# Kernel optimization log

Measured on AMD Instinct MI355X. Metric: run time of the kernel, lower is better.

The kernel has to match this reference:

```python
import jax, jax.numpy as jnp
import numpy as np
from math import ceil, log2

LEVELS = 6
N = 4096
DB4 = np.array([0.23037781330885523, 0.7148465705525415, 0.6308807679295904,
                -0.02798376941698385, -0.18703481171888114, 0.030841381835986965,
                0.032883011666982945, -0.010597401784997278], dtype=np.float32)


def setup_inputs() -> dict:
    key = jax.random.key(0)
    x = jax.random.normal(key, (N, N), dtype=jnp.float32)
    # learned filter bank: scaling.repeat(levels*2, 1)
    scaling = jnp.tile(jnp.asarray(DB4), (LEVELS * 2, 1))
    return {
        "x": x,
        "scaling": scaling,
        "alpha": jnp.float32(10.0),
        "b_plus": jnp.float32(2.0),
        "b_minus": jnp.float32(1.0),
    }


def compute_wavelet(h):
    # g_k = flip(h); odd indices negated
    g = jnp.flip(h, -1)
    sign = jnp.where(jnp.arange(g.shape[-1]) % 2 == 1, -1.0, 1.0).astype(g.dtype)
    return g * sign


def convolve(x, f, transpose=False):
    # circular convolution (or correlation if transpose) along last axis via FFT,
    # exactly as torch rfft/irfft with n=input_length
    L = x.shape[-1]
    fa = jnp.fft.rfft(x, axis=-1)
    fb = jnp.fft.rfft(f, n=L)
    if transpose:
        fb = jnp.conj(fb)
    return jnp.fft.irfft(fa * fb, n=L, axis=-1)


def forward_layer(x, h):
    w = compute_wavelet(h)
    return convolve(x, w)[:, ::2], convolve(x, h)[:, ::2]


def backward_layer(d, a, h):
    w = compute_wavelet(h)
    fd = jnp.zeros((d.shape[0], d.shape[1] * 2), d.dtype).at[:, ::2].set(d)
    fa = jnp.zeros((a.shape[0], a.shape[1] * 2), a.dtype).at[:, ::2].set(a)
    return convolve(fd, w, transpose=True) + convolve(fa, h, transpose=True)


def forward2d(x, hH, hV):
    d, a = forward_layer(x, hH)
    hh, hl = forward_layer(d.T, hV)
    hh, hl = hh.T, hl.T
    lh, ll = forward_layer(a.T, hV)
    lh, ll = lh.T, ll.T
    return (hh, hl, lh), ll


def backward2d(hh, hl, lh, ll, hH, hV):
    h = backward_layer(hh.T, hl.T, hV).T
    l = backward_layer(lh.T, ll.T, hV).T
    return backward_layer(h, l, hH)


def _despawn(x, scaling, alpha, b_plus, b_minus):
    n, m = x.shape
    pn = 2 ** ceil(log2(n)) - n
    pm = 2 ** ceil(log2(m)) - m
    xp = jnp.pad(x, ((0, pn), (0, pm)), mode="edge") if (pn or pm) else x

    approx = xp
    coeffs = []
    for lev in range(LEVELS):
        dets, approx = forward2d(approx, scaling[lev], scaling[lev + 1])
        coeffs.append(dets)

    def thr(t):
        return t * (jax.nn.sigmoid(alpha * (t - b_plus)) + jax.nn.sigmoid(-alpha * (t + b_minus)))

    filt = [tuple(thr(c) for c in tup) for tup in coeffs] + [thr(approx)]

    a = filt[-1]
    for lev in reversed(range(LEVELS)):
        hh, hl, lh = filt[lev]
        a = backward2d(hh, hl, lh, a, scaling[lev], scaling[lev + 1])

    flat = jnp.concatenate(
        [jnp.concatenate(tup, axis=-1).reshape(-1) for tup in filt[:-1]]
        + [filt[-1].reshape(-1)]
    )
    return a[:n, :m], flat


def reference(x, scaling, alpha, b_plus, b_minus):
    return _despawn(x, scaling, alpha, b_plus, b_minus)
```

## Files before the change

kernel.cpp:

```cpp
#include <hip/hip_runtime.h>
#include <hip/hip_bf16.h>


__device__ __forceinline__ float thrf(float t, float alpha, float bp, float bm) {
    float s1 = 1.0f / (1.0f + __expf(-alpha * (t - bp)));
    float s2 = 1.0f / (1.0f + __expf( alpha * (t + bm)));
    return t * (s1 + s2);
}

__device__ __forceinline__ void load_filt(const float* __restrict__ filt,
                                          float (&h)[8], float (&w)[8]) {
#pragma unroll
    for (int k = 0; k < 8; ++k) h[k] = filt[k];
#pragma unroll
    for (int k = 0; k < 8; ++k) w[k] = (k & 1) ? -h[7 - k] : h[7 - k];
}

__global__ __launch_bounds__(256) void fwd_fused(
    const float* __restrict__ X, int s, int sh,
    float* __restrict__ flat, float* __restrict__ All,
    const float* __restrict__ filt_row, const float* __restrict__ filt_col,
    const float* __restrict__ ap, const float* __restrict__ bpp,
    const float* __restrict__ bmp) {
    __shared__ float xs[72][73];
    __shared__ float Ds[72][33];
    __shared__ float As[72][33];
    const int tid = threadIdx.x;
    const int j0 = blockIdx.x * 32, i0 = blockIdx.y * 32;
    float hr[8], wr[8], hc[8], wc[8];
    load_filt(filt_row, hr, wr);
    load_filt(filt_col, hc, wc);
    const int sm = s - 1;
    for (int idx = tid; idx < 72 * 72; idx += 256) {
        int rr = idx / 72, cc = idx - rr * 72;
        int gr = (2 * i0 - 7 + rr) & sm;
        int gc = (2 * j0 - 7 + cc) & sm;
        xs[rr][cc] = X[(size_t)gr * s + gc];
    }
    __syncthreads();
    for (int idx = tid; idx < 72 * 32; idx += 256) {
        int rr = idx >> 5, j = idx & 31;
        float d = 0.f, a = 0.f;
#pragma unroll
        for (int k = 0; k < 8; ++k) {
            float v = xs[rr][2 * j + 7 - k];
            d += wr[k] * v;
            a += hr[k] * v;
        }
        Ds[rr][j] = d;
        As[rr][j] = a;
    }
    __syncthreads();
    const float alpha = *ap, bp = *bpp, bm = *bmp;
    for (int idx = tid; idx < 32 * 32; idx += 256) {
        int i = idx >> 5, j = idx & 31;
        float hh = 0.f, hl = 0.f, lh = 0.f, ll = 0.f;
#pragma unroll
        for (int k = 0; k < 8; ++k) {
            float dv = Ds[2 * i + 7 - k][j];
            float av = As[2 * i + 7 - k][j];
            hh += wc[k] * dv;
            hl += hc[k] * dv;
            lh += wc[k] * av;
            ll += hc[k] * av;
        }
        size_t ro = (size_t)(i0 + i) * (3 * sh) + (j0 + j);
        flat[ro]          = thrf(hh, alpha, bp, bm);
        flat[ro + sh]     = thrf(hl, alpha, bp, bm);
        flat[ro + 2 * sh] = thrf(lh, alpha, bp, bm);
        All[(size_t)(i0 + i) * sh + (j0 + j)] = ll;
    }
}

__global__ void thr_kernel(const float* __restrict__ in, float* __restrict__ out,
                           int n, const float* __restrict__ ap,
                           const float* __restrict__ bpp,
                           const float* __restrict__ bmp) {
    int idx = blockIdx.x * blockDim.x + threadIdx.x;
    if (idx >= n) return;
    out[idx] = thrf(in[idx], *ap, *bpp, *bmp);
}

__global__ __launch_bounds__(256) void inv_fused(
    const float* __restrict__ flatl, const float* __restrict__ a, int astride,
    int sc, float* __restrict__ outp, int ostride,
    const float* __restrict__ filt_col, const float* __restrict__ filt_row) {
    __shared__ float hhs[36][37], hls[36][37], lhs[36][37], as_[36][37];
    __shared__ float Hs[64][37], Ls[64][37];
    const int tid = threadIdx.x;
    const int m0 = blockIdx.x * 64, i0 = blockIdx.y * 64;
    float hr[8], wr[8], hc[8], wc[8];
    load_filt(filt_row, hr, wr);
    load_filt(filt_col, hc, wc);
    const int mm = sc - 1;
    const int r0 = i0 >> 1, c0 = m0 >> 1;
    const int ds = 3 * sc;
    for (int idx = tid; idx < 36 * 36; idx += 256) {
        int rr = idx / 36, cc = idx - rr * 36;
        int gr = (r0 + rr) & mm;
        int gc = (c0 + cc) & mm;
        size_t fo = (size_t)gr * ds + gc;
        hhs[rr][cc] = flatl[fo];
        hls[rr][cc] = flatl[fo + sc];
        lhs[rr][cc] = flatl[fo + 2 * sc];
        as_[rr][cc] = a[(size_t)gr * astride + gc];
    }
    __syncthreads();
    for (int idx = tid; idx < 64 * 36; idx += 256) {
        int n = idx / 36, jj = idx - (idx / 36) * 36;
        int nh = n >> 1;
        float Hv = 0.f, Lv = 0.f;
        if ((n & 1) == 0) {
#pragma unroll
            for (int t = 0; t < 4; ++t) {
                int lr = nh + t;
                Hv += wc[2 * t] * hhs[lr][jj] + hc[2 * t] * hls[lr][jj];
                Lv += wc[2 * t] * lhs[lr][jj] + hc[2 * t] * as_[lr][jj];
            }
        } else {
#pragma unroll
            for (int t = 0; t < 4; ++t) {
                int lr = nh + t + 1;
                Hv += wc[2 * t + 1] * hhs[lr][jj] + hc[2 * t + 1] * hls[lr][jj];
                Lv += wc[2 * t + 1] * lhs[lr][jj] + hc[2 * t + 1] * as_[lr][jj];
            }
        }
        Hs[n][jj] = Hv;
        Ls[n][jj] = Lv;
    }
    __syncthreads();
    for (int idx = tid; idx < 64 * 64; idx += 256) {
        int i = idx >> 6, m = idx & 63;
        int mh = m >> 1;
        float acc = 0.f;
        if ((m & 1) == 0) {
#pragma unroll
            for (int t = 0; t < 4; ++t) {
                int lc = mh + t;
                acc += wr[2 * t] * Hs[i][lc] + hr[2 * t] * Ls[i][lc];
            }
        } else {
#pragma unroll
            for (int t = 0; t < 4; ++t) {
                int lc = mh + t + 1;
                acc += wr[2 * t + 1] * Hs[i][lc] + hr[2 * t + 1] * Ls[i][lc];
            }
        }
        outp[(size_t)(i0 + i) * ostride + (m0 + m)] = acc;
    }
}

extern "C" void kernel_launch(void* const* d_in, const int* in_sizes, int n_in,
                              void* d_out, int out_size, void* d_ws, size_t ws_size,
                              hipStream_t stream) {
    const float* x    = (const float*)d_in[0];
    const float* scal = (const float*)d_in[1];
    const float* ap   = (const float*)d_in[2];
    const float* bp   = (const float*)d_in[3];
    const float* bm   = (const float*)d_in[4];
    float* out = (float*)d_out;
    float* ws  = (float*)d_ws;

    const int N = 4096;
    float* recon = out;
    float* flat  = out + 16777216;

    static const size_t Aoff[7] = {0, 0, 4194304, 5242880, 5505024, 5570560, 5586944};
    static const size_t flatOff[6] = {0, 12582912, 15728640, 16515072, 16711680, 16760832};
    const size_t finalOff = 16773120;
    float* P0 = ws + 5591040;
    float* P1 = ws + 5591040 + 4194304;

    dim3 blk(256);

    const float* src = x;
    for (int lev = 0; lev < 6; ++lev) {
        int s = N >> lev, sh = s >> 1;
        dim3 g(sh / 32, sh / 32);
        fwd_fused<<<g, blk, 0, stream>>>(src, s, sh, flat + flatOff[lev],
                                         ws + Aoff[lev + 1],
                                         scal + lev * 8, scal + (lev + 1) * 8,
                                         ap, bp, bm);
        src = ws + Aoff[lev + 1];
    }
    thr_kernel<<<dim3(16), blk, 0, stream>>>(ws + Aoff[6], flat + finalOff, 4096,
                                             ap, bp, bm);

    const float* a_in = flat + finalOff;
    for (int lev = 5; lev >= 0; --lev) {
        int sc = N >> (lev + 1), r = 2 * sc;
        float* outp = (lev == 0) ? recon : ((lev & 1) ? P1 : P0);
        dim3 g(r / 64, r / 64);
        inv_fused<<<g, blk, 0, stream>>>(flat + flatOff[lev], a_in, sc,
                                         sc, outp, r,
                                         scal + (lev + 1) * 8, scal + lev * 8);
        a_in = outp;
    }
}
```

Measured before the change: 340.9 us.

## Vectorize shared-memory staging and register-block filter stages in wavelet kernels

Both the forward and inverse fused kernels now load tiles from global memory with float4 accesses and trim the halo to aligned widths. Each thread now computes several adjacent outputs from one register window instead of one output per thread, which cuts redundant shared-memory reads. The inverse kernel's final stage writes float4 outputs. Removing the +1 padding may introduce LDS bank conflicts on the column-wise reads, and alignment of float4 global loads relies on the block offsets being multiples of four.

```diff
diff --git a/kernel.cpp b/kernel.cpp
--- a/kernel.cpp
+++ b/kernel.cpp
@@ -1,5 +1,4 @@
 #include <hip/hip_runtime.h>
-#include <hip/hip_bf16.h>
 
 
 __device__ __forceinline__ float thrf(float t, float alpha, float bp, float bm) {
@@ -22,53 +21,78 @@
     const float* __restrict__ filt_row, const float* __restrict__ filt_col,
     const float* __restrict__ ap, const float* __restrict__ bpp,
     const float* __restrict__ bmp) {
-    __shared__ float xs[72][73];
-    __shared__ float Ds[72][33];
-    __shared__ float As[72][33];
+    __shared__ __align__(16) float xs[70][72];
+    __shared__ __align__(16) float Ds[70][36];
+    __shared__ __align__(16) float As[70][36];
     const int tid = threadIdx.x;
     const int j0 = blockIdx.x * 32, i0 = blockIdx.y * 32;
     float hr[8], wr[8], hc[8], wc[8];
     load_filt(filt_row, hr, wr);
     load_filt(filt_col, hc, wc);
     const int sm = s - 1;
-    for (int idx = tid; idx < 72 * 72; idx += 256) {
-        int rr = idx / 72, cc = idx - rr * 72;
+
+    for (int idx = tid; idx < 70 * 18; idx += 256) {
+        int rr = idx / 18, c = idx - rr * 18;
         int gr = (2 * i0 - 7 + rr) & sm;
-        int gc = (2 * j0 - 7 + cc) & sm;
-        xs[rr][cc] = X[(size_t)gr * s + gc];
-    }
-    __syncthreads();
-    for (int idx = tid; idx < 72 * 32; idx += 256) {
-        int rr = idx >> 5, j = idx & 31;
-        float d = 0.f, a = 0.f;
-#pragma unroll
-        for (int k = 0; k < 8; ++k) {
-            float v = xs[rr][2 * j + 7 - k];
-            d += wr[k] * v;
-            a += hr[k] * v;
-        }
-        Ds[rr][j] = d;
-        As[rr][j] = a;
-    }
-    __syncthreads();
+        int gc = (2 * j0 - 8 + 4 * c) & sm;
+        *(float4*)&xs[rr][4 * c] = *(const float4*)&X[(size_t)gr * s + gc];
+    }
+    __syncthreads();
+
+    for (int idx = tid; idx < 70 * 8; idx += 256) {
+        int rr = idx >> 3, q = idx & 7;
+        const float4* xr = (const float4*)&xs[rr][8 * q];
+        float wv[16];
+#pragma unroll
+        for (int m = 0; m < 4; ++m) {
+            float4 t = xr[m];
+            wv[4 * m + 0] = t.x; wv[4 * m + 1] = t.y;
+            wv[4 * m + 2] = t.z; wv[4 * m + 3] = t.w;
+        }
+        float d[4], a[4];
+#pragma unroll
+        for (int e = 0; e < 4; ++e) {
+            float dd = 0.f, aa = 0.f;
+#pragma unroll
+            for (int u = 0; u < 8; ++u) {
+                float v = wv[2 * e + 1 + u];
+                dd += wr[7 - u] * v;
+                aa += hr[7 - u] * v;
+            }
+            d[e] = dd; a[e] = aa;
+        }
+        *(float4*)&Ds[rr][4 * q] = make_float4(d[0], d[1], d[2], d[3]);
+        *(float4*)&As[rr][4 * q] = make_float4(a[0], a[1], a[2], a[3]);
+    }
+    __syncthreads();
+
     const float alpha = *ap, bp = *bpp, bm = *bmp;
-    for (int idx = tid; idx < 32 * 32; idx += 256) {
-        int i = idx >> 5, j = idx & 31;
-        float hh = 0.f, hl = 0.f, lh = 0.f, ll = 0.f;
-#pragma unroll
-        for (int k = 0; k < 8; ++k) {
-            float dv = Ds[2 * i + 7 - k][j];
-            float av = As[2 * i + 7 - k][j];
-            hh += wc[k] * dv;
-            hl += hc[k] * dv;
-            lh += wc[k] * av;
-            ll += hc[k] * av;
-        }
-        size_t ro = (size_t)(i0 + i) * (3 * sh) + (j0 + j);
-        flat[ro]          = thrf(hh, alpha, bp, bm);
-        flat[ro + sh]     = thrf(hl, alpha, bp, bm);
-        flat[ro + 2 * sh] = thrf(lh, alpha, bp, bm);
-        All[(size_t)(i0 + i) * sh + (j0 + j)] = ll;
+    {
+        const int j = tid & 31, iq = tid >> 5;
+        float Dw[14], Aw[14];
+#pragma unroll
+        for (int t = 0; t < 14; ++t) {
+            Dw[t] = Ds[8 * iq + t][j];
+            Aw[t] = As[8 * iq + t][j];
+        }
+#pragma unroll
+        for (int e = 0; e < 4; ++e) {
+            float hh = 0.f, hl = 0.f, lh = 0.f, ll = 0.f;
+#pragma unroll
+            for (int u = 0; u < 8; ++u) {
+                float dv = Dw[2 * e + u], av = Aw[2 * e + u];
+                hh += wc[7 - u] * dv;
+                hl += hc[7 - u] * dv;
+                lh += wc[7 - u] * av;
+                ll += hc[7 - u] * av;
+            }
+            int row = i0 + 4 * iq + e;
+            size_t ro = (size_t)row * (3 * sh) + (j0 + j);
+            flat[ro]           = thrf(hh, alpha, bp, bm);
+            flat[ro + sh]      = thrf(hl, alpha, bp, bm);
+            flat[ro + 2 * sh]  = thrf(lh, alpha, bp, bm);
+            All[(size_t)row * sh + (j0 + j)] = ll;
+        }
     }
 }
 
@@ -85,8 +109,8 @@
     const float* __restrict__ flatl, const float* __restrict__ a, int astride,
     int sc, float* __restrict__ outp, int ostride,
     const float* __restrict__ filt_col, const float* __restrict__ filt_row) {
-    __shared__ float hhs[36][37], hls[36][37], lhs[36][37], as_[36][37];
-    __shared__ float Hs[64][37], Ls[64][37];
+    __shared__ __align__(16) float hhs[36][36], hls[36][36], lhs[36][36], as_[36][36];
+    __shared__ __align__(16) float Hs[64][36], Ls[64][36];
     const int tid = threadIdx.x;
     const int m0 = blockIdx.x * 64, i0 = blockIdx.y * 64;
     float hr[8], wr[8], hc[8], wc[8];
@@ -95,58 +119,76 @@
     const int mm = sc - 1;
     const int r0 = i0 >> 1, c0 = m0 >> 1;
     const int ds = 3 * sc;
-    for (int idx = tid; idx < 36 * 36; idx += 256) {
-        int rr = idx / 36, cc = idx - rr * 36;
+
+    for (int idx = tid; idx < 4 * 324; idx += 256) {
+        int aid = idx / 324, rem = idx - aid * 324;
+        int rr = rem / 9, c = rem - rr * 9;
         int gr = (r0 + rr) & mm;
-        int gc = (c0 + cc) & mm;
-        size_t fo = (size_t)gr * ds + gc;
-        hhs[rr][cc] = flatl[fo];
-        hls[rr][cc] = flatl[fo + sc];
-        lhs[rr][cc] = flatl[fo + 2 * sc];
-        as_[rr][cc] = a[(size_t)gr * astride + gc];
-    }
-    __syncthreads();
-    for (int idx = tid; idx < 64 * 36; idx += 256) {
-        int n = idx / 36, jj = idx - (idx / 36) * 36;
-        int nh = n >> 1;
-        float Hv = 0.f, Lv = 0.f;
-        if ((n & 1) == 0) {
-#pragma unroll
-            for (int t = 0; t < 4; ++t) {
-                int lr = nh + t;
-                Hv += wc[2 * t] * hhs[lr][jj] + hc[2 * t] * hls[lr][jj];
-                Lv += wc[2 * t] * lhs[lr][jj] + hc[2 * t] * as_[lr][jj];
-            }
-        } else {
-#pragma unroll
-            for (int t = 0; t < 4; ++t) {
-                int lr = nh + t + 1;
-                Hv += wc[2 * t + 1] * hhs[lr][jj] + hc[2 * t + 1] * hls[lr][jj];
-                Lv += wc[2 * t + 1] * lhs[lr][jj] + hc[2 * t + 1] * as_[lr][jj];
-            }
-        }
-        Hs[n][jj] = Hv;
-        Ls[n][jj] = Lv;
-    }
-    __syncthreads();
-    for (int idx = tid; idx < 64 * 64; idx += 256) {
-        int i = idx >> 6, m = idx & 63;
-        int mh = m >> 1;
-        float acc = 0.f;
-        if ((m & 1) == 0) {
-#pragma unroll
-            for (int t = 0; t < 4; ++t) {
-                int lc = mh + t;
-                acc += wr[2 * t] * Hs[i][lc] + hr[2 * t] * Ls[i][lc];
-            }
-        } else {
-#pragma unroll
-            for (int t = 0; t < 4; ++t) {
-                int lc = mh + t + 1;
-                acc += wr[2 * t + 1] * Hs[i][lc] + hr[2 * t + 1] * Ls[i][lc];
-            }
-        }
-        outp[(size_t)(i0 + i) * ostride + (m0 + m)] = acc;
+        int gc = (c0 + 4 * c) & mm;
+        if (aid == 0)
+            *(float4*)&hhs[rr][4 * c] = *(const float4*)&flatl[(size_t)gr * ds + gc];
+        else if (aid == 1)
+            *(float4*)&hls[rr][4 * c] = *(const float4*)&flatl[(size_t)gr * ds + sc + gc];
+        else if (aid == 2)
+            *(float4*)&lhs[rr][4 * c] = *(const float4*)&flatl[(size_t)gr * ds + 2 * sc + gc];
+        else
+            *(float4*)&as_[rr][4 * c] = *(const float4*)&a[(size_t)gr * astride + gc];
+    }
+    __syncthreads();
+
+    for (int idx = tid; idx < 16 * 36; idx += 256) {
+        int q = idx / 36, jj = idx - q * 36;
+        float hv[6], lv[6], gv[6], av[6];
+#pragma unroll
+        for (int d = 0; d < 6; ++d) {
+            int lr = 2 * q + d;
+            hv[d] = hhs[lr][jj];
+            lv[d] = hls[lr][jj];
+            gv[d] = lhs[lr][jj];
+            av[d] = as_[lr][jj];
+        }
+        float H0 = 0.f, H1 = 0.f, H2 = 0.f, H3 = 0.f;
+        float L0 = 0.f, L1 = 0.f, L2 = 0.f, L3 = 0.f;
+#pragma unroll
+        for (int t = 0; t < 4; ++t) {
+            float we = wc[2 * t], he = hc[2 * t];
+            float wo = wc[2 * t + 1], ho = hc[2 * t + 1];
+            H0 += we * hv[t]     + he * lv[t];
+            H1 += wo * hv[t + 1] + ho * lv[t + 1];
+            H2 += we * hv[t + 1] + he * lv[t + 1];
+            H3 += wo * hv[t + 2] + ho * lv[t + 2];
+            L0 += we * gv[t]     + he * av[t];
+            L1 += wo * gv[t + 1] + ho * av[t + 1];
+            L2 += we * gv[t + 1] + he * av[t + 1];
+            L3 += wo * gv[t + 2] + ho * av[t + 2];
+        }
+        Hs[4 * q + 0][jj] = H0; Hs[4 * q + 1][jj] = H1;
+        Hs[4 * q + 2][jj] = H2; Hs[4 * q + 3][jj] = H3;
+        Ls[4 * q + 0][jj] = L0; Ls[4 * q + 1][jj] = L1;
+        Ls[4 * q + 2][jj] = L2; Ls[4 * q + 3][jj] = L3;
+    }
+    __syncthreads();
+
+    for (int idx = tid; idx < 64 * 16; idx += 256) {
+        int i = idx >> 4, p = idx & 15;
+        const float2* hp = (const float2*)&Hs[i][2 * p];
+        const float2* lp = (const float2*)&Ls[i][2 * p];
+        float2 hA = hp[0], hB = hp[1], hC = hp[2];
+        float2 lA = lp[0], lB = lp[1], lC = lp[2];
+        float Hw[6] = {hA.x, hA.y, hB.x, hB.y, hC.x, hC.y};
+        float Lw[6] = {lA.x, lA.y, lB.x, lB.y, lC.x, lC.y};
+        float o0 = 0.f, o1 = 0.f, o2 = 0.f, o3 = 0.f;
+#pragma unroll
+        for (int t = 0; t < 4; ++t) {
+            float we = wr[2 * t], he = hr[2 * t];
+            float wo = wr[2 * t + 1], ho = hr[2 * t + 1];
+            o0 += we * Hw[t]     + he * Lw[t];
+            o1 += wo * Hw[t + 1] + ho * Lw[t + 1];
+            o2 += we * Hw[t + 1] + he * Lw[t + 1];
+            o3 += wo * Hw[t + 2] + ho * Lw[t + 2];
+        }
+        *(float4*)&outp[(size_t)(i0 + i) * ostride + (m0 + 4 * p)] =
+            make_float4(o0, o1, o2, o3);
     }
 }
 
```

Measured after the change: 307.0 us. -9.9%, faster.
